# Kernel tuning notes

Hardware: AMD Instinct MI355X
Metric: run time of the kernel (lower is better)

## Reference

```python
import jax, jax.numpy as jnp
import numpy as np

N, K, CIN, HID, COUT, E, MH = 8192, 200, 512, 256, 40, 5, 64
KG = K // E
EPS = 1e-5


def setup_inputs() -> dict:
    key = jax.random.key(0)
    ks = jax.random.split(key, 20)
    inp = {
        "X": jax.random.normal(ks[0], (N, CIN), jnp.float32),
        "La": jax.random.uniform(ks[1], (K,), jnp.float32),
        "U": jax.random.normal(ks[2], (N, K), jnp.float32),
        # 5 EigenExperts, each mlp = Linear(1,64) -> ReLU -> Linear(64,64) -> ReLU -> Linear(64,1)
        "eW1": jax.random.normal(ks[3], (E, MH), jnp.float32) * 0.5,
        "eb1": jax.random.normal(ks[4], (E, MH), jnp.float32) * 0.1,
        "eW2": jax.random.normal(ks[5], (E, MH, MH), jnp.float32) * (1.0 / np.sqrt(MH)),
        "eb2": jax.random.normal(ks[6], (E, MH), jnp.float32) * 0.1,
        "eW3": jax.random.normal(ks[7], (E, MH), jnp.float32) * (1.0 / np.sqrt(MH)),
        "eb3": jax.random.normal(ks[8], (E,), jnp.float32) * 0.1,
        # gate: Linear(5,5) -> ReLU -> Linear(5,5) -> Softmax
        "gW1": jax.random.normal(ks[9], (E, E), jnp.float32) * 0.4,
        "gb1": jax.random.normal(ks[10], (E,), jnp.float32) * 0.1,
        "gW2": jax.random.normal(ks[11], (E, E), jnp.float32) * 0.4,
        "gb2": jax.random.normal(ks[12], (E,), jnp.float32) * 0.1,
        # W: Linear(in_channels, hidden_dim)
        "Ww": jax.random.normal(ks[13], (CIN, HID), jnp.float32) * (1.0 / np.sqrt(CIN)),
        "Wb": jax.random.normal(ks[14], (HID,), jnp.float32) * 0.1,
        # BatchNorm1d(hidden_dim), training-mode batch stats
        "bn_gamma": jnp.ones((HID,), jnp.float32),
        "bn_beta": jnp.zeros((HID,), jnp.float32),
        # MLP: Linear(hidden_dim, out_channels)
        "Mw": jax.random.normal(ks[15], (HID, COUT), jnp.float32) * (1.0 / np.sqrt(HID)),
        "Mb": jax.random.normal(ks[16], (COUT,), jnp.float32) * 0.1,
    }
    return inp


def reference(X, La, U, eW1, eb1, eW2, eb2, eW3, eb3, gW1, gb1, gW2, gb2, Ww, Wb, bn_gamma, bn_beta, Mw, Mb):
    n, k = U.shape
    e = eW1.shape[0]
    kg = k // e
    # group eigenvector columns: U[:, i*kg:(i+1)*kg] for expert i -> [n, e, kg]
    Ue = U.reshape(n, e, kg)
    # EigenExpert tiny MLP applied elementwise over entries of each column, then mean over nodes
    h1 = jax.nn.relu(jnp.einsum('nek,eh->nekh', Ue, eW1) + eb1[None, :, None, :])
    h2 = jax.nn.relu(jnp.einsum('nekh,ehg->nekg', h1, eW2) + eb2[None, :, None, :])
    v = jnp.einsum('nekh,eh->nek', h2, eW3) + eb3[None, :, None]
    V = v.mean(axis=0)                      # [e, kg] importance per eigenvector
    # gate on per-group mean eigenvalue
    stats = La.reshape(e, kg).mean(axis=1)  # [e]
    g = jax.nn.relu(stats @ gW1 + gb1) @ gW2 + gb2
    g = jax.nn.softmax(g, axis=-1)          # [e]
    # sum_i g_i * U_i diag(V_i) U_i^T == (U * s) @ U^T with per-column scale s
    s = (g[:, None] * V).reshape(k)         # [k]
    A = (U * s[None, :]) @ U.T              # [n, n]
    out = A @ X                             # [n, cin]
    hidden = out @ Ww + Wb                  # [n, hid]
    mu = hidden.mean(axis=0)
    var = hidden.var(axis=0)                # biased, as torch BN uses for normalization
    h = (hidden - mu) * jax.lax.rsqrt(var + EPS) * bn_gamma + bn_beta
    h = jax.nn.relu(h)                      # dropout is identity (eval)
    logits = h @ Mw + Mb
    return jax.nn.log_softmax(logits, axis=1), hidden
```

## Files before the change

### kernel.cpp

```cpp
#include <hip/hip_runtime.h>
#include <hip/hip_bf16.h>

#define N_    8192
#define K_    200
#define CIN_  512
#define HID_  256
#define COUT_ 40
#define E_    5
#define MH_   64
#define KG_   40
#define EPS_  1e-5f

#define WS_VSUM  0
#define WS_BNSUM 256
#define WS_T     768
#define WS_S     103168
#define WS_G     103424

typedef __bf16 bf16x8 __attribute__((ext_vector_type(8)));
typedef float  f32x16 __attribute__((ext_vector_type(16)));

__device__ __forceinline__ uint packbf(float a, float b) {
    union { __bf16 h[2]; uint u; } p;
    p.h[0] = (__bf16)a; p.h[1] = (__bf16)b;
    return p.u;
}

union UB { uint4 q; bf16x8 v; };

__global__ __launch_bounds__(256) void k_expert(
    const float* __restrict__ U,
    const float* __restrict__ eW1, const float* __restrict__ eb1,
    const float* __restrict__ eW2, const float* __restrict__ eb2,
    const float* __restrict__ eW3, const float* __restrict__ eb3,
    float* __restrict__ Vsum)
{
    const int e   = blockIdx.x;
    const int tid = threadIdx.x;
    const int w   = tid >> 6;
    const int l   = tid & 63;
    const int lo  = l & 31;
    const int hi  = l >> 5;

    __shared__ float sW1[MH_], sb1[MH_], sb2s[MH_], sW3s[MH_];
    __shared__ float colsum[KG_];

    if (tid < MH_) {
        sW1[tid]  = eW1[e*MH_ + tid];
        sb1[tid]  = eb1[e*MH_ + tid];
        sb2s[tid] = eb2[e*MH_ + tid];
        sW3s[tid] = eW3[e*MH_ + tid];
    }
    if (tid < KG_) colsum[tid] = 0.f;
    const float b3 = eb3[e];

    bf16x8 fa[2][4];
    {
        const float* W2e = eW2 + e*MH_*MH_;
        #pragma unroll
        for (int mt = 0; mt < 2; ++mt) {
            const int grow = mt*32 + lo;
            #pragma unroll
            for (int t = 0; t < 4; ++t) {
                const int k0 = 16*t + 8*hi;
                union { uint u[4]; bf16x8 v; } fb;
                #pragma unroll
                for (int r = 0; r < 4; ++r) {
                    const float x0 = W2e[(k0+2*r  )*MH_ + grow];
                    const float x1 = W2e[(k0+2*r+1)*MH_ + grow];
                    fb.u[r] = packbf(x0, x1);
                }
                fa[mt][t] = fb.v;
            }
        }
    }
    __syncthreads();

    for (int it = 0; it < 4; ++it) {
        const int tile  = (blockIdx.y*16 + it*4 + w);
        const int elem0 = tile * 64;
        const int idx   = elem0 + l;
        const int n     = idx / KG_;
        const int kg    = idx - n*KG_;
        const float u   = U[n*K_ + e*KG_ + kg];

        const float ucol0 = __shfl(u, lo);
        const float ucol1 = __shfl(u, 32 + lo);

        f32x16 acc00 = {0}; f32x16 acc10 = {0};
        f32x16 acc01 = {0}; f32x16 acc11 = {0};
        #pragma unroll
        for (int t = 0; t < 4; ++t) {
            const int k0 = 16*t + 8*hi;
            float2 w1p[4], b1p[4];
            #pragma unroll
            for (int r = 0; r < 4; ++r) {
                w1p[r] = *reinterpret_cast<const float2*>(&sW1[k0 + 2*r]);
                b1p[r] = *reinterpret_cast<const float2*>(&sb1[k0 + 2*r]);
            }
            union { uint u[4]; bf16x8 v; } b0, b1;
            #pragma unroll
            for (int r = 0; r < 4; ++r) {
                const float pa = fmaxf(fmaf(ucol0, w1p[r].x, b1p[r].x), 0.f);
                const float pb = fmaxf(fmaf(ucol0, w1p[r].y, b1p[r].y), 0.f);
                b0.u[r] = packbf(pa, pb);
                const float qa = fmaxf(fmaf(ucol1, w1p[r].x, b1p[r].x), 0.f);
                const float qb = fmaxf(fmaf(ucol1, w1p[r].y, b1p[r].y), 0.f);
                b1.u[r] = packbf(qa, qb);
            }
            acc00 = __builtin_amdgcn_mfma_f32_32x32x16_bf16(fa[0][t], b0.v, acc00, 0, 0, 0);
            acc10 = __builtin_amdgcn_mfma_f32_32x32x16_bf16(fa[1][t], b0.v, acc10, 0, 0, 0);
            acc01 = __builtin_amdgcn_mfma_f32_32x32x16_bf16(fa[0][t], b1.v, acc01, 0, 0, 0);
            acc11 = __builtin_amdgcn_mfma_f32_32x32x16_bf16(fa[1][t], b1.v, acc11, 0, 0, 0);
        }

        float vs0 = 0.f, vs1 = 0.f;
        #pragma unroll
        for (int r = 0; r < 16; ++r) {
            const int gb  = (r & 3) + 8*(r >> 2) + 4*hi;
            const float b2a = sb2s[gb],      w3a = sW3s[gb];
            const float b2b = sb2s[32 + gb], w3b = sW3s[32 + gb];
            vs0 += fmaxf(acc00[r] + b2a, 0.f)*w3a + fmaxf(acc10[r] + b2b, 0.f)*w3b;
            vs1 += fmaxf(acc01[r] + b2a, 0.f)*w3a + fmaxf(acc11[r] + b2b, 0.f)*w3b;
        }
        vs0 += __shfl_xor(vs0, 32);
        vs1 += __shfl_xor(vs1, 32);

        const float myv    = (hi ? vs1 : vs0) + b3;
        const int   myelem = (hi ? 32 : 0) + lo;
        const int   mykg   = (elem0 + myelem) % KG_;
        atomicAdd(&colsum[mykg], myv);
    }

    __syncthreads();
    if (tid < KG_) atomicAdd(&Vsum[e*KG_ + tid], colsum[tid]);
}

__global__ void k_gate(
    const float* __restrict__ La,
    const float* __restrict__ gW1, const float* __restrict__ gb1,
    const float* __restrict__ gW2, const float* __restrict__ gb2,
    const float* __restrict__ Vsum, float* __restrict__ s)
{
    __shared__ float sg[E_];
    const int tid = threadIdx.x;
    if (tid == 0) {
        float stats[E_], g1[E_], g2[E_];
        for (int e = 0; e < E_; ++e) {
            float acc = 0.f;
            for (int k = 0; k < KG_; ++k) acc += La[e*KG_ + k];
            stats[e] = acc * (1.0f/KG_);
        }
        for (int j = 0; j < E_; ++j) {
            float acc = gb1[j];
            for (int i = 0; i < E_; ++i) acc += stats[i]*gW1[i*E_ + j];
            g1[j] = fmaxf(acc, 0.f);
        }
        float m = -1e30f;
        for (int j = 0; j < E_; ++j) {
            float acc = gb2[j];
            for (int i = 0; i < E_; ++i) acc += g1[i]*gW2[i*E_ + j];
            g2[j] = acc;
            m = fmaxf(m, acc);
        }
        float ssum = 0.f;
        for (int j = 0; j < E_; ++j) { g2[j] = expf(g2[j]-m); ssum += g2[j]; }
        for (int j = 0; j < E_; ++j) sg[j] = g2[j] / ssum;
    }
    __syncthreads();
    if (tid < K_) s[tid] = sg[tid / KG_] * Vsum[tid] * (1.0f/N_);
}

__global__ __launch_bounds__(256) void k_utx(
    const float* __restrict__ U, const float* __restrict__ X,
    float* __restrict__ T)
{
    const int c0    = blockIdx.x * 32;
    const int r0    = blockIdx.y * 128;
    const int mhalf = blockIdx.z;
    const int tid = threadIdx.x;
    const int w   = tid >> 6;
    const int l   = tid & 63;
    const int lo  = l & 31;
    const int hi  = l >> 5;

    const int mt   = mhalf*4 + w;
    const int colc = min(32*mt + lo, K_ - 1);
    const int xcol = c0 + lo;

    f32x16 acc = {0};
    #pragma unroll
    for (int s = 0; s < 8; ++s) {
        const int kr = r0 + 16*s + 8*hi;
        union { uint u[4]; bf16x8 v; } ax, bx;
        #pragma unroll
        for (int j2 = 0; j2 < 4; ++j2) {
            const float ua = U[(kr + 2*j2    )*K_ + colc];
            const float ub = U[(kr + 2*j2 + 1)*K_ + colc];
            ax.u[j2] = packbf(ua, ub);
            const float xa = X[(kr + 2*j2    )*CIN_ + xcol];
            const float xb = X[(kr + 2*j2 + 1)*CIN_ + xcol];
            bx.u[j2] = packbf(xa, xb);
        }
        acc = __builtin_amdgcn_mfma_f32_32x32x16_bf16(ax.v, bx.v, acc, 0, 0, 0);
    }

    #pragma unroll
    for (int r = 0; r < 16; ++r) {
        const int mm = 32*mt + (r & 3) + 8*(r >> 2) + 4*hi;
        if (mm < K_)
            atomicAdd(&T[mm*CIN_ + c0 + lo], acc[r]);
    }
}

__global__ __launch_bounds__(256) void k_g(
    const float* __restrict__ T, const float* __restrict__ Ww,
    float* __restrict__ G)
{
    const int k0  = blockIdx.x * 4;
    const int c   = threadIdx.x;
    __shared__ float4 sT4[4][128];

    for (int j = threadIdx.x; j < 512; j += 256) {
        const int r = j >> 7, c4 = j & 127;
        sT4[r][c4] = reinterpret_cast<const float4*>(T)[(k0+r)*128 + c4];
    }
    __syncthreads();

    float a0 = 0.f, a1 = 0.f, a2 = 0.f, a3 = 0.f;
    for (int ci4 = 0; ci4 < 128; ++ci4) {
        const float w0 = Ww[(4*ci4+0)*HID_ + c];
        const float w1 = Ww[(4*ci4+1)*HID_ + c];
        const float w2 = Ww[(4*ci4+2)*HID_ + c];
        const float w3 = Ww[(4*ci4+3)*HID_ + c];
        float4 t;
        t = sT4[0][ci4]; a0 += t.x*w0 + t.y*w1 + t.z*w2 + t.w*w3;
        t = sT4[1][ci4]; a1 += t.x*w0 + t.y*w1 + t.z*w2 + t.w*w3;
        t = sT4[2][ci4]; a2 += t.x*w0 + t.y*w1 + t.z*w2 + t.w*w3;
        t = sT4[3][ci4]; a3 += t.x*w0 + t.y*w1 + t.z*w2 + t.w*w3;
    }
    G[(k0+0)*HID_ + c] = a0;
    G[(k0+1)*HID_ + c] = a1;
    G[(k0+2)*HID_ + c] = a2;
    G[(k0+3)*HID_ + c] = a3;
}

__global__ __launch_bounds__(256) void k_hidden(
    const float* __restrict__ U, const float* __restrict__ s,
    const float* __restrict__ G, const float* __restrict__ Wb,
    float* __restrict__ hid)
{
    const int c0  = blockIdx.x * 64;
    const int n0  = blockIdx.y * 128;
    const int tid = threadIdx.x;
    const int w   = tid >> 6;
    const int l   = tid & 63;
    const int lo  = l & 31;
    const int hi  = l >> 5;

    __shared__ uint  spkA[104][128];
    __shared__ uint  spkB[104][64];
    __shared__ float ss[K_];

    if (tid < K_) ss[tid] = s[tid];
    __syncthreads();

    for (int j = tid; j < 128*26; j += 256) {
        const int m = j & 127, g = j >> 7;
        uint4 pk = make_uint4(0u, 0u, 0u, 0u);
        if (g < 25) {
            const float4 a = *reinterpret_cast<const float4*>(&U[(n0+m)*K_ + 8*g]);
            const float4 b = *reinterpret_cast<const float4*>(&U[(n0+m)*K_ + 8*g + 4]);
            pk.x = packbf(a.x*ss[8*g+0], a.y*ss[8*g+1]);
            pk.y = packbf(a.z*ss[8*g+2], a.w*ss[8*g+3]);
            pk.z = packbf(b.x*ss[8*g+4], b.y*ss[8*g+5]);
            pk.w = packbf(b.z*ss[8*g+6], b.w*ss[8*g+7]);
        }
        spkA[4*g+0][m] = pk.x;
        spkA[4*g+1][m] = pk.y;
        spkA[4*g+2][m] = pk.z;
        spkA[4*g+3][m] = pk.w;
    }
    for (int j = tid; j < 64*26; j += 256) {
        const int c = j & 63, g = j >> 6;
        uint4 pk = make_uint4(0u, 0u, 0u, 0u);
        if (g < 25) {
            const float v0 = G[(8*g+0)*HID_ + c0+c], v1 = G[(8*g+1)*HID_ + c0+c];
            const float v2 = G[(8*g+2)*HID_ + c0+c], v3 = G[(8*g+3)*HID_ + c0+c];
            const float v4 = G[(8*g+4)*HID_ + c0+c], v5 = G[(8*g+5)*HID_ + c0+c];
            const float v6 = G[(8*g+6)*HID_ + c0+c], v7 = G[(8*g+7)*HID_ + c0+c];
            pk.x = packbf(v0, v1); pk.y = packbf(v2, v3);
            pk.z = packbf(v4, v5); pk.w = packbf(v6, v7);
        }
        spkB[4*g+0][c] = pk.x;
        spkB[4*g+1][c] = pk.y;
        spkB[4*g+2][c] = pk.z;
        spkB[4*g+3][c] = pk.w;
    }
    __syncthreads();

    f32x16 acc0 = {0}, acc1 = {0};
    #pragma unroll
    for (int t = 0; t < 13; ++t) {
        const int kp = 8*t + 4*hi;
        union { uint u[4]; bf16x8 v; } fa;
        fa.u[0] = spkA[kp+0][32*w + lo];
        fa.u[1] = spkA[kp+1][32*w + lo];
        fa.u[2] = spkA[kp+2][32*w + lo];
        fa.u[3] = spkA[kp+3][32*w + lo];
        UB b0, b1;
        b0.q.x = spkB[kp+0][lo];      b0.q.y = spkB[kp+1][lo];
        b0.q.z = spkB[kp+2][lo];      b0.q.w = spkB[kp+3][lo];
        b1.q.x = spkB[kp+0][32 + lo]; b1.q.y = spkB[kp+1][32 + lo];
        b1.q.z = spkB[kp+2][32 + lo]; b1.q.w = spkB[kp+3][32 + lo];
        acc0 = __builtin_amdgcn_mfma_f32_32x32x16_bf16(fa.v, b0.v, acc0, 0, 0, 0);
        acc1 = __builtin_amdgcn_mfma_f32_32x32x16_bf16(fa.v, b1.v, acc1, 0, 0, 0);
    }

    const float wb0 = Wb[c0 + lo], wb1 = Wb[c0 + 32 + lo];
    #pragma unroll
    for (int r = 0; r < 16; ++r) {
        const int row = 32*w + (r & 3) + 8*(r >> 2) + 4*hi;
        hid[(n0+row)*HID_ + c0 + lo]      = acc0[r] + wb0;
        hid[(n0+row)*HID_ + c0 + 32 + lo] = acc1[r] + wb1;
    }
}

__global__ __launch_bounds__(256) void k_bnstat(
    const float* __restrict__ hid, float* __restrict__ bnsum)
{
    const int c  = threadIdx.x;
    const int n0 = blockIdx.x * 32;
    float sm = 0.f, sq = 0.f;
    for (int r = 0; r < 32; ++r) {
        const float v = hid[(n0+r)*HID_ + c];
        sm += v; sq += v*v;
    }
    atomicAdd(&bnsum[c], sm);
    atomicAdd(&bnsum[HID_ + c], sq);
}

__global__ __launch_bounds__(256) void k_logits(
    const float* __restrict__ hid, const float* __restrict__ bnsum,
    const float* __restrict__ gamma, const float* __restrict__ beta,
    const float* __restrict__ Mw, const float* __restrict__ Mb,
    float* __restrict__ outls)
{
    __shared__ float sc[HID_], sh[HID_], sMb[COUT_];
    __shared__ float sMw[HID_][COUT_];
    __shared__ float sPart[8][32][41];

    const int tid = threadIdx.x;
    const int r   = tid & 31;
    const int sl  = tid >> 5;

    {
        const float sm = bnsum[tid], sq = bnsum[HID_+tid];
        const float mu  = sm * (1.0f/N_);
        const float var = sq * (1.0f/N_) - mu*mu;
        const float a   = gamma[tid] * rsqrtf(var + EPS_);
        sc[tid] = a;
        sh[tid] = beta[tid] - mu*a;
    }
    for (int j = tid; j < HID_*COUT_/4; j += 256)
        reinterpret_cast<float4*>(&sMw[0][0])[j] = reinterpret_cast<const float4*>(Mw)[j];
    if (tid < COUT_) sMb[tid] = Mb[tid];
    __syncthreads();

    const int n  = blockIdx.x*32 + r;
    const int cb = sl * 32;
    float acc[COUT_];
    #pragma unroll
    for (int j = 0; j < COUT_; ++j) acc[j] = 0.f;

    const float4* hrow = reinterpret_cast<const float4*>(&hid[n*HID_ + cb]);
    #pragma unroll
    for (int c4 = 0; c4 < 8; ++c4) {
        const float4 h4 = hrow[c4];
        const float hv[4] = {h4.x, h4.y, h4.z, h4.w};
        #pragma unroll
        for (int q = 0; q < 4; ++q) {
            const int c = cb + 4*c4 + q;
            const float hn = fmaxf(hv[q]*sc[c] + sh[c], 0.f);
            #pragma unroll
            for (int j0 = 0; j0 < COUT_; j0 += 4) {
                const float4 wv = *reinterpret_cast<const float4*>(&sMw[c][j0]);
                acc[j0+0] += hn*wv.x; acc[j0+1] += hn*wv.y;
                acc[j0+2] += hn*wv.z; acc[j0+3] += hn*wv.w;
            }
        }
    }
    #pragma unroll
    for (int j = 0; j < COUT_; ++j) sPart[sl][r][j] = acc[j];
    __syncthreads();

    if (tid < 32) {
        const int n2 = blockIdx.x*32 + tid;
        float a2[COUT_];
        #pragma unroll
        for (int j = 0; j < COUT_; ++j) {
            float sum = sMb[j];
            #pragma unroll
            for (int s2 = 0; s2 < 8; ++s2) sum += sPart[s2][tid][j];
            a2[j] = sum;
        }
        float m = -1e30f;
        #pragma unroll
        for (int j = 0; j < COUT_; ++j) m = fmaxf(m, a2[j]);
        float ssum = 0.f;
        #pragma unroll
        for (int j = 0; j < COUT_; ++j) ssum += expf(a2[j] - m);
        const float lse = m + logf(ssum);
        #pragma unroll
        for (int j = 0; j < COUT_; ++j)
            outls[n2*COUT_ + j] = a2[j] - lse;
    }
}

extern "C" void kernel_launch(void* const* d_in, const int* in_sizes, int n_in,
                              void* d_out, int out_size, void* d_ws, size_t ws_size,
                              hipStream_t stream)
{
    const float* X        = (const float*)d_in[0];
    const float* La       = (const float*)d_in[1];
    const float* U        = (const float*)d_in[2];
    const float* eW1      = (const float*)d_in[3];
    const float* eb1      = (const float*)d_in[4];
    const float* eW2      = (const float*)d_in[5];
    const float* eb2      = (const float*)d_in[6];
    const float* eW3      = (const float*)d_in[7];
    const float* eb3      = (const float*)d_in[8];
    const float* gW1      = (const float*)d_in[9];
    const float* gb1      = (const float*)d_in[10];
    const float* gW2      = (const float*)d_in[11];
    const float* gb2      = (const float*)d_in[12];
    const float* Ww       = (const float*)d_in[13];
    const float* Wb       = (const float*)d_in[14];
    const float* bn_gamma = (const float*)d_in[15];
    const float* bn_beta  = (const float*)d_in[16];
    const float* Mw       = (const float*)d_in[17];
    const float* Mb       = (const float*)d_in[18];

    float* out   = (float*)d_out;
    float* ws    = (float*)d_ws;
    float* Vsum  = ws + WS_VSUM;
    float* bnsum = ws + WS_BNSUM;
    float* T     = ws + WS_T;
    float* s     = ws + WS_S;
    float* G     = ws + WS_G;

    float* outls = out;
    float* hid   = out + N_*COUT_;

    hipMemsetAsync(ws, 0, (size_t)(WS_T + K_*CIN_) * sizeof(float), stream);

    k_utx   <<<dim3(16, 64, 2), 256, 0, stream>>>(U, X, T);
    k_expert<<<dim3(E_, 320),   256, 0, stream>>>(U, eW1, eb1, eW2, eb2, eW3, eb3, Vsum);
    k_gate  <<<1,   256, 0, stream>>>(La, gW1, gb1, gW2, gb2, Vsum, s);
    k_g     <<<50,  256, 0, stream>>>(T, Ww, G);
    k_hidden<<<dim3(4, 64), 256, 0, stream>>>(U, s, G, Wb, hid);
    k_bnstat<<<256, 256, 0, stream>>>(hid, bnsum);
    k_logits<<<256, 256, 0, stream>>>(hid, bnsum, bn_gamma, bn_beta, Mw, Mb, outls);
}
```

Before: 235.8 us.

## Restructure U^T X with LDS tiling and split-K buffers, fuse BN stats, fp16 expert MLP

```diff
diff --git a/kernel.cpp b/kernel.cpp
--- a/kernel.cpp
+++ b/kernel.cpp
@@ -18,6 +18,8 @@
 #define WS_G     103424
 
 typedef __bf16 bf16x8 __attribute__((ext_vector_type(8)));
+typedef _Float16 f16x2 __attribute__((ext_vector_type(2)));
+typedef _Float16 f16x8 __attribute__((ext_vector_type(8)));
 typedef float  f32x16 __attribute__((ext_vector_type(16)));
 
 __device__ __forceinline__ uint packbf(float a, float b) {
@@ -27,6 +29,7 @@
 }
 
 union UB { uint4 q; bf16x8 v; };
+union UHF { f16x2 h2[4]; f16x8 v; };
 
 __global__ __launch_bounds__(256) void k_expert(
     const float* __restrict__ U,
@@ -42,19 +45,24 @@
     const int lo  = l & 31;
     const int hi  = l >> 5;
 
-    __shared__ float sW1[MH_], sb1[MH_], sb2s[MH_], sW3s[MH_];
+    __shared__ f16x2 sW1h[32], sb1h[32];
+    __shared__ float sb2s[MH_], sW3s[MH_];
     __shared__ float colsum[KG_];
 
+    if (tid < 32) {
+        f16x2 w2; w2.x = (_Float16)eW1[e*MH_ + 2*tid]; w2.y = (_Float16)eW1[e*MH_ + 2*tid + 1];
+        sW1h[tid] = w2;
+        f16x2 b2; b2.x = (_Float16)eb1[e*MH_ + 2*tid]; b2.y = (_Float16)eb1[e*MH_ + 2*tid + 1];
+        sb1h[tid] = b2;
+    }
     if (tid < MH_) {
-        sW1[tid]  = eW1[e*MH_ + tid];
-        sb1[tid]  = eb1[e*MH_ + tid];
         sb2s[tid] = eb2[e*MH_ + tid];
         sW3s[tid] = eW3[e*MH_ + tid];
     }
     if (tid < KG_) colsum[tid] = 0.f;
     const float b3 = eb3[e];
 
-    bf16x8 fa[2][4];
+    UHF fa[2][4];
     {
         const float* W2e = eW2 + e*MH_*MH_;
         #pragma unroll
@@ -63,55 +71,57 @@
             #pragma unroll
             for (int t = 0; t < 4; ++t) {
                 const int k0 = 16*t + 8*hi;
-                union { uint u[4]; bf16x8 v; } fb;
                 #pragma unroll
                 for (int r = 0; r < 4; ++r) {
-                    const float x0 = W2e[(k0+2*r  )*MH_ + grow];
-                    const float x1 = W2e[(k0+2*r+1)*MH_ + grow];
-                    fb.u[r] = packbf(x0, x1);
+                    f16x2 p;
+                    p.x = (_Float16)W2e[(k0+2*r  )*MH_ + grow];
+                    p.y = (_Float16)W2e[(k0+2*r+1)*MH_ + grow];
+                    fa[mt][t].h2[r] = p;
                 }
-                fa[mt][t] = fb.v;
             }
         }
     }
     __syncthreads();
 
+    float uu[4]; int kgs[4];
+    {
+        const int idx0 = (blockIdx.y*16 + w)*64 + l;
+        int n = idx0 / KG_, kg = idx0 - n*KG_;
+        #pragma unroll
+        for (int it = 0; it < 4; ++it) {
+            uu[it]  = U[n*K_ + e*KG_ + kg];
+            kgs[it] = kg;
+            kg += 16; if (kg >= KG_) { kg -= KG_; n += 1; }
+            n += 6;
+        }
+    }
+
+    const f16x2 z2 = {(_Float16)0.f, (_Float16)0.f};
+
+    #pragma unroll
     for (int it = 0; it < 4; ++it) {
-        const int tile  = (blockIdx.y*16 + it*4 + w);
-        const int elem0 = tile * 64;
-        const int idx   = elem0 + l;
-        const int n     = idx / KG_;
-        const int kg    = idx - n*KG_;
-        const float u   = U[n*K_ + e*KG_ + kg];
-
-        const float ucol0 = __shfl(u, lo);
-        const float ucol1 = __shfl(u, 32 + lo);
+        const float ucol0 = __shfl(uu[it], lo);
+        const float ucol1 = __shfl(uu[it], 32 + lo);
+        f16x2 u20; u20.x = (_Float16)ucol0; u20.y = (_Float16)ucol0;
+        f16x2 u21; u21.x = (_Float16)ucol1; u21.y = (_Float16)ucol1;
 
         f32x16 acc00 = {0}; f32x16 acc10 = {0};
         f32x16 acc01 = {0}; f32x16 acc11 = {0};
         #pragma unroll
         for (int t = 0; t < 4; ++t) {
-            const int k0 = 16*t + 8*hi;
-            float2 w1p[4], b1p[4];
+            const int kp = 8*t + 4*hi;
+            UHF b0, b1;
             #pragma unroll
             for (int r = 0; r < 4; ++r) {
-                w1p[r] = *reinterpret_cast<const float2*>(&sW1[k0 + 2*r]);
-                b1p[r] = *reinterpret_cast<const float2*>(&sb1[k0 + 2*r]);
+                const f16x2 w1  = sW1h[kp + r];
+                const f16x2 b1c = sb1h[kp + r];
+                b0.h2[r] = __builtin_elementwise_max(u20*w1 + b1c, z2);
+                b1.h2[r] = __builtin_elementwise_max(u21*w1 + b1c, z2);
             }
-            union { uint u[4]; bf16x8 v; } b0, b1;
-            #pragma unroll
-            for (int r = 0; r < 4; ++r) {
-                const float pa = fmaxf(fmaf(ucol0, w1p[r].x, b1p[r].x), 0.f);
-                const float pb = fmaxf(fmaf(ucol0, w1p[r].y, b1p[r].y), 0.f);
-                b0.u[r] = packbf(pa, pb);
-                const float qa = fmaxf(fmaf(ucol1, w1p[r].x, b1p[r].x), 0.f);
-                const float qb = fmaxf(fmaf(ucol1, w1p[r].y, b1p[r].y), 0.f);
-                b1.u[r] = packbf(qa, qb);
-            }
-            acc00 = __builtin_amdgcn_mfma_f32_32x32x16_bf16(fa[0][t], b0.v, acc00, 0, 0, 0);
-            acc10 = __builtin_amdgcn_mfma_f32_32x32x16_bf16(fa[1][t], b0.v, acc10, 0, 0, 0);
-            acc01 = __builtin_amdgcn_mfma_f32_32x32x16_bf16(fa[0][t], b1.v, acc01, 0, 0, 0);
-            acc11 = __builtin_amdgcn_mfma_f32_32x32x16_bf16(fa[1][t], b1.v, acc11, 0, 0, 0);
+            acc00 = __builtin_amdgcn_mfma_f32_32x32x16_f16(fa[0][t].v, b0.v, acc00, 0, 0, 0);
+            acc10 = __builtin_amdgcn_mfma_f32_32x32x16_f16(fa[1][t].v, b0.v, acc10, 0, 0, 0);
+            acc01 = __builtin_amdgcn_mfma_f32_32x32x16_f16(fa[0][t].v, b1.v, acc01, 0, 0, 0);
+            acc11 = __builtin_amdgcn_mfma_f32_32x32x16_f16(fa[1][t].v, b1.v, acc11, 0, 0, 0);
         }
 
         float vs0 = 0.f, vs1 = 0.f;
@@ -126,10 +136,8 @@
         vs0 += __shfl_xor(vs0, 32);
         vs1 += __shfl_xor(vs1, 32);
 
-        const float myv    = (hi ? vs1 : vs0) + b3;
-        const int   myelem = (hi ? 32 : 0) + lo;
-        const int   mykg   = (elem0 + myelem) % KG_;
-        atomicAdd(&colsum[mykg], myv);
+        const float myv = (hi ? vs1 : vs0) + b3;
+        atomicAdd(&colsum[kgs[it]], myv);
     }
 
     __syncthreads();
@@ -173,44 +181,103 @@
 
 __global__ __launch_bounds__(256) void k_utx(
     const float* __restrict__ U, const float* __restrict__ X,
-    float* __restrict__ T)
-{
-    const int c0    = blockIdx.x * 32;
-    const int r0    = blockIdx.y * 128;
-    const int mhalf = blockIdx.z;
+    float* __restrict__ P)
+{
+    const int nc0 = blockIdx.x * 64;
+    const int mc0 = blockIdx.y * 64;
+    const int ks  = blockIdx.z;
+    const int r0  = ks * 512;
     const int tid = threadIdx.x;
-    const int w   = tid >> 6;
-    const int l   = tid & 63;
-    const int lo  = l & 31;
-    const int hi  = l >> 5;
-
-    const int mt   = mhalf*4 + w;
-    const int colc = min(32*mt + lo, K_ - 1);
-    const int xcol = c0 + lo;
+    const int w   = tid >> 6, l = tid & 63, lo = l & 31, hi = l >> 5;
+    const int mq  = w >> 1, nq = w & 1;
+
+    __shared__ uint sU[2][32][68];
+    __shared__ uint sX[2][32][68];
+
+    const int rpA = tid >> 4;
+    const int rpB = rpA + 16;
+    const int c4  = tid & 15;
+    const int mcA = mc0 + 4*c4;
+    const int xcA = nc0 + 4*c4;
+    const int UMAX = N_*K_ - 4;
+
+    float4 uA0,uA1,uB0,uB1,xA0,xA1,xB0,xB1;
+
+#define UTX_LD(chunk) {                                                       \
+    const int rb_ = r0 + 64*(chunk);                                          \
+    uA0 = *reinterpret_cast<const float4*>(&U[min((rb_+2*rpA  )*K_ + mcA, UMAX)]); \
+    uA1 = *reinterpret_cast<const float4*>(&U[min((rb_+2*rpA+1)*K_ + mcA, UMAX)]); \
+    uB0 = *reinterpret_cast<const float4*>(&U[min((rb_+2*rpB  )*K_ + mcA, UMAX)]); \
+    uB1 = *reinterpret_cast<const float4*>(&U[min((rb_+2*rpB+1)*K_ + mcA, UMAX)]); \
+    xA0 = *reinterpret_cast<const float4*>(&X[(rb_+2*rpA  )*CIN_ + xcA]);     \
+    xA1 = *reinterpret_cast<const float4*>(&X[(rb_+2*rpA+1)*CIN_ + xcA]);     \
+    xB0 = *reinterpret_cast<const float4*>(&X[(rb_+2*rpB  )*CIN_ + xcA]);     \
+    xB1 = *reinterpret_cast<const float4*>(&X[(rb_+2*rpB+1)*CIN_ + xcA]); }
+
+#define UTX_WR(buf) {                                                         \
+    uint4 p_;                                                                 \
+    p_.x = packbf(uA0.x,uA1.x); p_.y = packbf(uA0.y,uA1.y);                   \
+    p_.z = packbf(uA0.z,uA1.z); p_.w = packbf(uA0.w,uA1.w);                   \
+    *reinterpret_cast<uint4*>(&sU[buf][rpA][4*c4]) = p_;                      \
+    p_.x = packbf(uB0.x,uB1.x); p_.y = packbf(uB0.y,uB1.y);                   \
+    p_.z = packbf(uB0.z,uB1.z); p_.w = packbf(uB0.w,uB1.w);                   \
+    *reinterpret_cast<uint4*>(&sU[buf][rpB][4*c4]) = p_;                      \
+    p_.x = packbf(xA0.x,xA1.x); p_.y = packbf(xA0.y,xA1.y);                   \
+    p_.z = packbf(xA0.z,xA1.z); p_.w = packbf(xA0.w,xA1.w);                   \
+    *reinterpret_cast<uint4*>(&sX[buf][rpA][4*c4]) = p_;                      \
+    p_.x = packbf(xB0.x,xB1.x); p_.y = packbf(xB0.y,xB1.y);                   \
+    p_.z = packbf(xB0.z,xB1.z); p_.w = packbf(xB0.w,xB1.w);                   \
+    *reinterpret_cast<uint4*>(&sX[buf][rpB][4*c4]) = p_; }
+
+#define UTX_MM(buf) {                                                         \
+    _Pragma("unroll") for (int ksi = 0; ksi < 4; ++ksi) {                     \
+        const int rp0_ = 8*ksi + 4*hi;                                        \
+        UB a_, b_;                                                            \
+        a_.q.x = sU[buf][rp0_+0][32*mq+lo];                                   \
+        a_.q.y = sU[buf][rp0_+1][32*mq+lo];                                   \
+        a_.q.z = sU[buf][rp0_+2][32*mq+lo];                                   \
+        a_.q.w = sU[buf][rp0_+3][32*mq+lo];                                   \
+        b_.q.x = sX[buf][rp0_+0][32*nq+lo];                                   \
+        b_.q.y = sX[buf][rp0_+1][32*nq+lo];                                   \
+        b_.q.z = sX[buf][rp0_+2][32*nq+lo];                                   \
+        b_.q.w = sX[buf][rp0_+3][32*nq+lo];                                   \
+        acc = __builtin_amdgcn_mfma_f32_32x32x16_bf16(a_.v, b_.v, acc, 0,0,0); } }
 
     f32x16 acc = {0};
-    #pragma unroll
-    for (int s = 0; s < 8; ++s) {
-        const int kr = r0 + 16*s + 8*hi;
-        union { uint u[4]; bf16x8 v; } ax, bx;
-        #pragma unroll
-        for (int j2 = 0; j2 < 4; ++j2) {
-            const float ua = U[(kr + 2*j2    )*K_ + colc];
-            const float ub = U[(kr + 2*j2 + 1)*K_ + colc];
-            ax.u[j2] = packbf(ua, ub);
-            const float xa = X[(kr + 2*j2    )*CIN_ + xcol];
-            const float xb = X[(kr + 2*j2 + 1)*CIN_ + xcol];
-            bx.u[j2] = packbf(xa, xb);
-        }
-        acc = __builtin_amdgcn_mfma_f32_32x32x16_bf16(ax.v, bx.v, acc, 0, 0, 0);
+    UTX_LD(0);
+    UTX_WR(0);
+    __syncthreads();
+    #pragma unroll
+    for (int t = 0; t < 8; ++t) {
+        if (t < 7) UTX_LD(t+1);
+        UTX_MM(t & 1);
+        if (t < 7) UTX_WR((t+1) & 1);
+        __syncthreads();
     }
 
     #pragma unroll
     for (int r = 0; r < 16; ++r) {
-        const int mm = 32*mt + (r & 3) + 8*(r >> 2) + 4*hi;
-        if (mm < K_)
-            atomicAdd(&T[mm*CIN_ + c0 + lo], acc[r]);
-    }
+        const int mrow = mc0 + mq*32 + (r & 3) + 8*(r >> 2) + 4*hi;
+        const int ncol = nc0 + nq*32 + lo;
+        P[(ks*256 + mrow)*512 + ncol] = acc[r];
+    }
+#undef UTX_LD
+#undef UTX_WR
+#undef UTX_MM
+}
+
+__global__ __launch_bounds__(256) void k_red(
+    const float* __restrict__ P, float* __restrict__ T)
+{
+    const int j  = blockIdx.x*256 + threadIdx.x;
+    const int m  = j >> 7;
+    const int c4 = j & 127;
+    float4 s4 = {0.f, 0.f, 0.f, 0.f};
+    for (int ks = 0; ks < 16; ++ks) {
+        const float4 v = *reinterpret_cast<const float4*>(&P[(ks*256 + m)*512 + 4*c4]);
+        s4.x += v.x; s4.y += v.y; s4.z += v.z; s4.w += v.w;
+    }
+    *reinterpret_cast<float4*>(&T[m*512 + 4*c4]) = s4;
 }
 
 __global__ __launch_bounds__(256) void k_g(
@@ -248,9 +315,9 @@
 __global__ __launch_bounds__(256) void k_hidden(
     const float* __restrict__ U, const float* __restrict__ s,
     const float* __restrict__ G, const float* __restrict__ Wb,
-    float* __restrict__ hid)
-{
-    const int c0  = blockIdx.x * 64;
+    float* __restrict__ hid, float* __restrict__ bnsum)
+{
+    const int c0  = blockIdx.x * 32;
     const int n0  = blockIdx.y * 128;
     const int tid = threadIdx.x;
     const int w   = tid >> 6;
@@ -258,86 +325,72 @@
     const int lo  = l & 31;
     const int hi  = l >> 5;
 
-    __shared__ uint  spkA[104][128];
-    __shared__ uint  spkB[104][64];
-    __shared__ float ss[K_];
-
-    if (tid < K_) ss[tid] = s[tid];
-    __syncthreads();
-
-    for (int j = tid; j < 128*26; j += 256) {
-        const int m = j & 127, g = j >> 7;
-        uint4 pk = make_uint4(0u, 0u, 0u, 0u);
-        if (g < 25) {
-            const float4 a = *reinterpret_cast<const float4*>(&U[(n0+m)*K_ + 8*g]);
-            const float4 b = *reinterpret_cast<const float4*>(&U[(n0+m)*K_ + 8*g + 4]);
-            pk.x = packbf(a.x*ss[8*g+0], a.y*ss[8*g+1]);
-            pk.y = packbf(a.z*ss[8*g+2], a.w*ss[8*g+3]);
-            pk.z = packbf(b.x*ss[8*g+4], b.y*ss[8*g+5]);
-            pk.w = packbf(b.z*ss[8*g+6], b.w*ss[8*g+7]);
-        }
-        spkA[4*g+0][m] = pk.x;
-        spkA[4*g+1][m] = pk.y;
-        spkA[4*g+2][m] = pk.z;
-        spkA[4*g+3][m] = pk.w;
-    }
-    for (int j = tid; j < 64*26; j += 256) {
-        const int c = j & 63, g = j >> 6;
-        uint4 pk = make_uint4(0u, 0u, 0u, 0u);
-        if (g < 25) {
-            const float v0 = G[(8*g+0)*HID_ + c0+c], v1 = G[(8*g+1)*HID_ + c0+c];
-            const float v2 = G[(8*g+2)*HID_ + c0+c], v3 = G[(8*g+3)*HID_ + c0+c];
-            const float v4 = G[(8*g+4)*HID_ + c0+c], v5 = G[(8*g+5)*HID_ + c0+c];
-            const float v6 = G[(8*g+6)*HID_ + c0+c], v7 = G[(8*g+7)*HID_ + c0+c];
-            pk.x = packbf(v0, v1); pk.y = packbf(v2, v3);
-            pk.z = packbf(v4, v5); pk.w = packbf(v6, v7);
-        }
-        spkB[4*g+0][c] = pk.x;
-        spkB[4*g+1][c] = pk.y;
-        spkB[4*g+2][c] = pk.z;
-        spkB[4*g+3][c] = pk.w;
-    }
-    __syncthreads();
-
-    f32x16 acc0 = {0}, acc1 = {0};
+    __shared__ uint  sA[104][129];
+    __shared__ uint  sB[104][33];
+    __shared__ float ss[208];
+
+    if (tid < 208) ss[tid] = (tid < K_) ? s[tid] : 0.f;
+    __syncthreads();
+
+    #pragma unroll
+    for (int u = 0; u < 13; ++u) {
+        const int j  = tid + u*256;
+        const int m  = j & 127, kq = j >> 7;
+        float4 a = {0,0,0,0}, b = {0,0,0,0};
+        if (kq < 25) {
+            a = *reinterpret_cast<const float4*>(&U[(n0+m)*K_ + 8*kq]);
+            b = *reinterpret_cast<const float4*>(&U[(n0+m)*K_ + 8*kq + 4]);
+            a.x *= ss[8*kq+0]; a.y *= ss[8*kq+1]; a.z *= ss[8*kq+2]; a.w *= ss[8*kq+3];
+            b.x *= ss[8*kq+4]; b.y *= ss[8*kq+5]; b.z *= ss[8*kq+6]; b.w *= ss[8*kq+7];
+        }
+        sA[4*kq+0][m] = packbf(a.x, a.y);
+        sA[4*kq+1][m] = packbf(a.z, a.w);
+        sA[4*kq+2][m] = packbf(b.x, b.y);
+        sA[4*kq+3][m] = packbf(b.z, b.w);
+    }
+    for (int j = tid; j < 832; j += 256) {
+        const int c = j & 31, kq = j >> 5;
+        float g[8];
+        #pragma unroll
+        for (int i = 0; i < 8; ++i)
+            g[i] = (kq < 25) ? G[(8*kq+i)*HID_ + c0 + c] : 0.f;
+        sB[4*kq+0][c] = packbf(g[0], g[1]);
+        sB[4*kq+1][c] = packbf(g[2], g[3]);
+        sB[4*kq+2][c] = packbf(g[4], g[5]);
+        sB[4*kq+3][c] = packbf(g[6], g[7]);
+    }
+    __syncthreads();
+
+    f32x16 acc = {0};
     #pragma unroll
     for (int t = 0; t < 13; ++t) {
-        const int kp = 8*t + 4*hi;
-        union { uint u[4]; bf16x8 v; } fa;
-        fa.u[0] = spkA[kp+0][32*w + lo];
-        fa.u[1] = spkA[kp+1][32*w + lo];
-        fa.u[2] = spkA[kp+2][32*w + lo];
-        fa.u[3] = spkA[kp+3][32*w + lo];
-        UB b0, b1;
-        b0.q.x = spkB[kp+0][lo];      b0.q.y = spkB[kp+1][lo];
-        b0.q.z = spkB[kp+2][lo];      b0.q.w = spkB[kp+3][lo];
-        b1.q.x = spkB[kp+0][32 + lo]; b1.q.y = spkB[kp+1][32 + lo];
-        b1.q.z = spkB[kp+2][32 + lo]; b1.q.w = spkB[kp+3][32 + lo];
-        acc0 = __builtin_amdgcn_mfma_f32_32x32x16_bf16(fa.v, b0.v, acc0, 0, 0, 0);
-        acc1 = __builtin_amdgcn_mfma_f32_32x32x16_bf16(fa.v, b1.v, acc1, 0, 0, 0);
-    }
-
-    const float wb0 = Wb[c0 + lo], wb1 = Wb[c0 + 32 + lo];
+        const int rp0 = 8*t + 4*hi;
+        UB a_, b_;
+        a_.q.x = sA[rp0+0][32*w + lo];
+        a_.q.y = sA[rp0+1][32*w + lo];
+        a_.q.z = sA[rp0+2][32*w + lo];
+        a_.q.w = sA[rp0+3][32*w + lo];
+        b_.q.x = sB[rp0+0][lo];
+        b_.q.y = sB[rp0+1][lo];
+        b_.q.z = sB[rp0+2][lo];
+        b_.q.w = sB[rp0+3][lo];
+        acc = __builtin_amdgcn_mfma_f32_32x32x16_bf16(a_.v, b_.v, acc, 0, 0, 0);
+    }
+
+    const float wb = Wb[c0 + lo];
+    float sm = 0.f, sq = 0.f;
     #pragma unroll
     for (int r = 0; r < 16; ++r) {
         const int row = 32*w + (r & 3) + 8*(r >> 2) + 4*hi;
-        hid[(n0+row)*HID_ + c0 + lo]      = acc0[r] + wb0;
-        hid[(n0+row)*HID_ + c0 + 32 + lo] = acc1[r] + wb1;
-    }
-}
-
-__global__ __launch_bounds__(256) void k_bnstat(
-    const float* __restrict__ hid, float* __restrict__ bnsum)
-{
-    const int c  = threadIdx.x;
-    const int n0 = blockIdx.x * 32;
-    float sm = 0.f, sq = 0.f;
-    for (int r = 0; r < 32; ++r) {
-        const float v = hid[(n0+r)*HID_ + c];
-        sm += v; sq += v*v;
-    }
-    atomicAdd(&bnsum[c], sm);
-    atomicAdd(&bnsum[HID_ + c], sq);
+        const float h = acc[r] + wb;
+        hid[(n0+row)*HID_ + c0 + lo] = h;
+        sm += h; sq += h*h;
+    }
+    sm += __shfl_xor(sm, 32); sq += __shfl_xor(sq, 32);
+    if (hi == 0) {
+        atomicAdd(&bnsum[c0 + lo],        sm);
+        atomicAdd(&bnsum[HID_ + c0 + lo], sq);
+    }
 }
 
 __global__ __launch_bounds__(256) void k_logits(
@@ -451,14 +504,15 @@
 
     float* outls = out;
     float* hid   = out + N_*COUT_;
-
-    hipMemsetAsync(ws, 0, (size_t)(WS_T + K_*CIN_) * sizeof(float), stream);
-
-    k_utx   <<<dim3(16, 64, 2), 256, 0, stream>>>(U, X, T);
-    k_expert<<<dim3(E_, 320),   256, 0, stream>>>(U, eW1, eb1, eW2, eb2, eW3, eb3, Vsum);
+    float* P     = out;
+
+    (void)hipMemsetAsync(ws, 0, (size_t)768 * sizeof(float), stream);
+
+    k_utx   <<<dim3(8, 4, 16), 256, 0, stream>>>(U, X, P);
+    k_expert<<<dim3(E_, 320),  256, 0, stream>>>(U, eW1, eb1, eW2, eb2, eW3, eb3, Vsum);
     k_gate  <<<1,   256, 0, stream>>>(La, gW1, gb1, gW2, gb2, Vsum, s);
+    k_red   <<<100, 256, 0, stream>>>(P, T);
     k_g     <<<50,  256, 0, stream>>>(T, Ww, G);
-    k_hidden<<<dim3(4, 64), 256, 0, stream>>>(U, s, G, Wb, hid);
-    k_bnstat<<<256, 256, 0, stream>>>(hid, bnsum);
+    k_hidden<<<dim3(8, 64), 256, 0, stream>>>(U, s, G, Wb, hid, bnsum);
     k_logits<<<256, 256, 0, stream>>>(hid, bnsum, bn_gamma, bn_beta, Mw, Mb, outls);
 }
```

Measured after the change: 228.1 us. 1.03x faster.
